# Performance work log

Measured on AMD Instinct MI355X. Metric: run time of the kernel, lower is better.

The kernel has to match this reference:

```python
import jax, jax.numpy as jnp
import numpy as np

HEADS = 16
D_MODEL = 1024
GROUP = 4
SEQ = 2048
HEAD_DIM = D_MODEL // HEADS          # 64
KV_HEADS = HEADS // GROUP            # 4


def rope_tables(head_dim, seq_len, base=10000.0):
    # NOTE: faithful to source: exp = -2*arange(0,d,2)/d  (steps of 2 -> base^{-4j/d})
    exp = -2.0 * jnp.arange(0, head_dim, 2, dtype=jnp.float32) / head_dim
    thetas = jnp.power(base, exp)                       # [d/2]
    m = jnp.arange(seq_len, dtype=jnp.float32)          # [S]
    freq = jnp.outer(m, thetas)                         # [S, d/2]
    return jnp.cos(freq), jnp.sin(freq)


def apply_rope(x, cos, sin):
    # x: [B,S,H,D]; complex rotation on consecutive pairs
    B, S, H, D = x.shape
    xr = x.reshape(B, S, H, D // 2, 2)
    x0, x1 = xr[..., 0], xr[..., 1]
    c = cos[None, :S, None, :]
    s = sin[None, :S, None, :]
    out = jnp.stack([x0 * c - x1 * s, x0 * s + x1 * c], axis=-1)
    return out.reshape(B, S, H, D)


def setup_inputs() -> dict:
    key = jax.random.key(0)
    ks = jax.random.split(key, 8)
    B = 1
    q = jax.random.normal(ks[0], (B, SEQ, D_MODEL), dtype=jnp.float32)
    k = jax.random.normal(ks[1], (B, SEQ, D_MODEL), dtype=jnp.float32)
    v = jax.random.normal(ks[2], (B, SEQ, D_MODEL), dtype=jnp.float32)
    mask = jnp.tril(jnp.ones((SEQ, SEQ), dtype=jnp.int32))[None]  # causal [B,S,S]
    sc = 0.02
    Wq = jax.random.normal(ks[3], (D_MODEL, D_MODEL), dtype=jnp.float32) * sc
    Wk = jax.random.normal(ks[4], (D_MODEL, D_MODEL // GROUP), dtype=jnp.float32) * sc
    Wv = jax.random.normal(ks[5], (D_MODEL, D_MODEL // GROUP), dtype=jnp.float32) * sc
    Wo = jax.random.normal(ks[6], (D_MODEL, D_MODEL), dtype=jnp.float32) * sc
    bq = jnp.zeros((D_MODEL,), jnp.float32)
    bk = jnp.zeros((D_MODEL // GROUP,), jnp.float32)
    bv = jnp.zeros((D_MODEL // GROUP,), jnp.float32)
    bo = jnp.zeros((D_MODEL,), jnp.float32)
    return {"q": q, "k": k, "v": v, "mask": mask, "Wq": Wq, "bq": bq,
            "Wk": Wk, "bk": bk, "Wv": Wv, "bv": bv, "Wo": Wo, "bo": bo}


def reference(q, k, v, mask, Wq, bq, Wk, bk, Wv, bv, Wo, bo):
    B, S, _ = q.shape
    cos, sin = rope_tables(HEAD_DIM, S)
    qh = (q @ Wq + bq).reshape(B, S, HEADS, HEAD_DIM)
    kh = (k @ Wk + bk).reshape(B, S, KV_HEADS, HEAD_DIM)
    vh = (v @ Wv + bv).reshape(B, S, KV_HEADS, HEAD_DIM)
    qh = apply_rope(qh, cos, sin)
    kh = apply_rope(kh, cos, sin)
    qh = qh.transpose(0, 2, 1, 3)                       # [B,H,S,D]
    kh = kh.transpose(0, 2, 1, 3)                       # [B,Hkv,S,D]
    vh = vh.transpose(0, 2, 1, 3)
    # torch .repeat tiles: query head j attends kv head j % KV_HEADS
    kh = jnp.tile(kh, (1, GROUP, 1, 1))                 # [B,H,S,D]
    vh = jnp.tile(vh, (1, GROUP, 1, 1))
    scores = jnp.einsum('bhqd,bhkd->bhqk', qh, kh) / jnp.sqrt(
        jnp.asarray(HEAD_DIM, dtype=qh.dtype))
    scores = jnp.where(mask[:, None, :, :] == 0, -jnp.inf, scores)
    attn = jax.nn.softmax(scores, axis=-1)
    out = jnp.einsum('bhqk,bhkd->bhqd', attn, vh)
    out = out.transpose(0, 2, 1, 3).reshape(B, S, D_MODEL)
    return out @ Wo + bo
```

## Files before the change

kernel.cpp:

```cpp
#include <hip/hip_runtime.h>
#include <hip/hip_bf16.h>
#include <math.h>


#define SEQ 2048
#define DM 1024
#define HD 64

using u16 = unsigned short;
typedef __attribute__((ext_vector_type(8))) short bf16x8;
typedef __attribute__((ext_vector_type(4))) float f32x4;

#define QSCALE 0.18033688011112042f

__device__ __forceinline__ u16 f2b(float f) {
    union { float f; unsigned int i; } v; v.f = f;
    unsigned int u = v.i;
    return (u16)((u + 0x7fffu + ((u >> 16) & 1u)) >> 16);
}
__device__ __forceinline__ u16 f2b_fast(float f) {
    union { float f; unsigned int i; } v; v.f = f;
    return (u16)((v.i + 0x8000u) >> 16);
}

__global__ __launch_bounds__(256) void prep_kernel(
    const float* __restrict__ qin, const float* __restrict__ kin, const float* __restrict__ vin,
    const float* __restrict__ Wq, const float* __restrict__ Wk,
    const float* __restrict__ Wv, const float* __restrict__ Wo,
    u16* __restrict__ Xq, u16* __restrict__ Xk, u16* __restrict__ Xv,
    u16* __restrict__ Wt, u16* __restrict__ wot, float2* __restrict__ rope)
{
    const int b = blockIdx.x;
    const int t = threadIdx.x;

    if (b < 640) {
        __shared__ short T[64][72];
        const float* W; u16* dst; int N, t0, rowoff;
        if (b < 256)      { W = Wq; dst = Wt;  N = 1024; t0 = b;       rowoff = 0; }
        else if (b < 320) { W = Wk; dst = Wt;  N = 256;  t0 = b - 256; rowoff = 1024; }
        else if (b < 384) { W = Wv; dst = Wt;  N = 256;  t0 = b - 320; rowoff = 1280; }
        else              { W = Wo; dst = wot; N = 1024; t0 = b - 384; rowoff = 0; }
        const int ntn = N >> 6;
        const int k0 = (t0 / ntn) * 64, n0 = (t0 % ntn) * 64;
        const int r = t >> 4, c4 = (t & 15) * 4;
        #pragma unroll
        for (int rr = 0; rr < 4; ++rr) {
            const int k = r + rr * 16;
            float4 w4 = *reinterpret_cast<const float4*>(W + (size_t)(k0 + k) * N + n0 + c4);
            T[c4 + 0][k] = (short)f2b(w4.x);
            T[c4 + 1][k] = (short)f2b(w4.y);
            T[c4 + 2][k] = (short)f2b(w4.z);
            T[c4 + 3][k] = (short)f2b(w4.w);
        }
        __syncthreads();
        const int n = t >> 2, ck = (t & 3) * 16;
        if (b < 384) {
            const int nt = (rowoff + n0) >> 6, kt = k0 >> 6;
            char* dp = (char*)(dst + (size_t)(nt * 16 + kt) * 4096) + n * 128;
            const int g0 = (t & 3) * 2, rx = n & 7;
            *reinterpret_cast<bf16x8*>(dp + (((g0    ) ^ rx) << 4)) =
                *reinterpret_cast<const bf16x8*>(&T[n][ck]);
            *reinterpret_cast<bf16x8*>(dp + (((g0 + 1) ^ rx) << 4)) =
                *reinterpret_cast<const bf16x8*>(&T[n][ck + 8]);
        } else {
            u16* dp = dst + (size_t)(n0 + n) * DM + k0 + ck;
            *reinterpret_cast<bf16x8*>(dp)     = *reinterpret_cast<const bf16x8*>(&T[n][ck]);
            *reinterpret_cast<bf16x8*>(dp + 8) = *reinterpret_cast<const bf16x8*>(&T[n][ck + 8]);
        }
    } else if (b < 1408) {
        const int idx = b - 640;
        const int which = idx >> 8;
        const int ib = idx & 255;
        const float* src = (which == 0) ? qin : (which == 1) ? kin : vin;
        u16* dst = (which == 0) ? Xq : (which == 1) ? Xk : Xv;
        const int m  = ib * 8 + (t >> 5);
        const int mt = m >> 6, r = m & 63, rx = r & 7;
        const int col0 = (t & 31) * 32;
        const float* sp = src + (size_t)m * 1024 + col0;
        #pragma unroll
        for (int c = 0; c < 4; ++c) {
            float4 x0 = *reinterpret_cast<const float4*>(sp + c * 8);
            float4 x1 = *reinterpret_cast<const float4*>(sp + c * 8 + 4);
            bf16x8 o;
            o[0] = (short)f2b(x0.x); o[1] = (short)f2b(x0.y);
            o[2] = (short)f2b(x0.z); o[3] = (short)f2b(x0.w);
            o[4] = (short)f2b(x1.x); o[5] = (short)f2b(x1.y);
            o[6] = (short)f2b(x1.z); o[7] = (short)f2b(x1.w);
            const int col = col0 + c * 8;
            const int kt = col >> 6, g = (col & 63) >> 3;
            char* dp = (char*)(dst + (size_t)(mt * 16 + kt) * 4096)
                     + r * 128 + ((g ^ rx) << 4);
            *reinterpret_cast<bf16x8*>(dp) = o;
        }
    } else {
        const int m = (b - 1408) * 256 + t;
        float2* rp = rope + (size_t)m * 32;
        for (int pi = 0; pi < 32; ++pi) {
            const float theta = exp2f(-0.8304820237f * (float)pi);
            float sn, cs;
            sincosf((float)m * theta, &sn, &cs);
            rp[pi] = make_float2(cs, sn);
        }
    }
}

__global__ __launch_bounds__(256) void proj_mfma(
    const u16* __restrict__ Xq, const u16* __restrict__ Xk, const u16* __restrict__ Xv,
    const u16* __restrict__ Wt,
    const float* __restrict__ bq, const float* __restrict__ bk, const float* __restrict__ bv,
    const float2* __restrict__ rope,
    u16* __restrict__ Qr, u16* __restrict__ Kr, u16* __restrict__ Vrt)
{
    const int n0 = blockIdx.x * 64, m0 = blockIdx.y * 64;
    const int zone = (n0 < 1024) ? 0 : (n0 < 1280) ? 1 : 2;
    const u16* __restrict__ Az = (zone == 0) ? Xq : (zone == 1) ? Xk : Xv;

    __shared__ __align__(16) u16 As[2][4096];
    __shared__ __align__(16) u16 Bs[2][4096];

    const int t = threadIdx.x;
    const int w = t >> 6, lane = t & 63, lm = lane & 15, quad = lane >> 4;

    f32x4 acc[4] = { {0,0,0,0}, {0,0,0,0}, {0,0,0,0}, {0,0,0,0} };

    const char* Ag = (const char*)(Az + (size_t)(m0 >> 6) * 16 * 4096);
    const char* Bg = (const char*)(Wt + (size_t)(n0 >> 6) * 16 * 4096);

    auto stage = [&](int bufi, int kti) {
        const char* gA = Ag + (size_t)kti * 8192 + w * 2048 + lane * 16;
        const char* gB = Bg + (size_t)kti * 8192 + w * 2048 + lane * 16;
        char* lA = (char*)&As[bufi][0] + w * 2048;
        char* lB = (char*)&Bs[bufi][0] + w * 2048;
        #pragma unroll
        for (int i = 0; i < 2; ++i) {
            __builtin_amdgcn_global_load_lds(
                (const __attribute__((address_space(1))) unsigned int*)(gA + i * 1024),
                (__attribute__((address_space(3))) unsigned int*)(lA + i * 1024), 16, 0, 0);
            __builtin_amdgcn_global_load_lds(
                (const __attribute__((address_space(1))) unsigned int*)(gB + i * 1024),
                (__attribute__((address_space(3))) unsigned int*)(lB + i * 1024), 16, 0, 0);
        }
    };

    stage(0, 0);
    __syncthreads();

    const int rA = 16 * w + lm;
    const int axr = rA & 7;
    for (int kt = 0; kt < 16; ++kt) {
        const int buf = kt & 1;
        if (kt < 15) stage(buf ^ 1, kt + 1);
        const char* Ab = (const char*)&As[buf][0];
        const char* Bb = (const char*)&Bs[buf][0];
        bf16x8 af0 = *reinterpret_cast<const bf16x8*>(Ab + rA * 128 + (((quad    ) ^ axr) << 4));
        bf16x8 af1 = *reinterpret_cast<const bf16x8*>(Ab + rA * 128 + (((4 | quad) ^ axr) << 4));
        #pragma unroll
        for (int nb = 0; nb < 4; ++nb) {
            const int rB = 16 * nb + lm, bxr = rB & 7;
            bf16x8 b0 = *reinterpret_cast<const bf16x8*>(Bb + rB * 128 + (((quad    ) ^ bxr) << 4));
            bf16x8 b1 = *reinterpret_cast<const bf16x8*>(Bb + rB * 128 + (((4 | quad) ^ bxr) << 4));
            acc[nb] = __builtin_amdgcn_mfma_f32_16x16x32_bf16(af0, b0, acc[nb], 0, 0, 0);
            acc[nb] = __builtin_amdgcn_mfma_f32_16x16x32_bf16(af1, b1, acc[nb], 0, 0, 0);
        }
        __syncthreads();
    }

    const float* __restrict__ bias = (zone == 0) ? bq : (zone == 1) ? bk : bv;
    const int nbase = (zone == 0) ? n0 : (zone == 1) ? (n0 - 1024) : (n0 - 1280);
    const int head = nbase >> 6;
    #pragma unroll
    for (int nb = 0; nb < 4; ++nb) {
        const int d = 16 * nb + lm;
        const float bvv = bias[nbase + d];
        float vals[4];
        #pragma unroll
        for (int r = 0; r < 4; ++r) vals[r] = acc[nb][r] + bvv;
        if (zone != 2) {
            const int pi = d >> 1;
            const bool odd = (lm & 1);
            const float sca = (zone == 0) ? QSCALE : 1.0f;
            u16* op = (zone == 0 ? Qr : Kr) + (size_t)head * SEQ * HD;
            #pragma unroll
            for (int r = 0; r < 4; ++r) {
                const int m = m0 + 16 * w + quad * 4 + r;
                const float2 cs2 = rope[(size_t)m * 32 + pi];
                float x  = vals[r];
                float xp = __shfl_xor(x, 1);
                float o  = (odd ? (xp * cs2.y + x * cs2.x)
                                : (x * cs2.x - xp * cs2.y)) * sca;
                op[(size_t)m * HD + d] = f2b(o);
            }
        } else {
            u16* vp = Vrt + ((size_t)head * HD + d) * SEQ;
            #pragma unroll
            for (int r = 0; r < 4; ++r) {
                const int m = m0 + 16 * w + quad * 4 + r;
                const int within = m & 63;
                const int pos = (m & ~63) + 4 * (within & 15) + (within >> 4);
                vp[pos] = f2b(vals[r]);
            }
        }
    }
}

__global__ __launch_bounds__(256) void attn_mfma(
    const u16* __restrict__ Qr, const u16* __restrict__ Kr, const u16* __restrict__ Vrt,
    u16* __restrict__ AO)
{
    const int bid = blockIdx.x;
    const int h  = bid & 15;
    const int qt = (bid < 256) ? (bid >> 4) : 31 - ((bid - 256) >> 4);
    const int kvh = h & 3;

    __shared__ u16 Ks[2][64][72];
    __shared__ u16 Vt[2][64][72];
    __shared__ u16 Ps[4][16][76];

    const int t = threadIdx.x;
    const int w = t >> 6, lane = t & 63, lm = lane & 15, quad = lane >> 4;

    {
        const int row = lane >> 2, c = (lane & 3) * 16;
        const u16* qp = Qr + ((size_t)h * SEQ + qt * 64 + w * 16 + row) * HD + c;
        *reinterpret_cast<bf16x8*>(&Ps[w][row][c])     = *reinterpret_cast<const bf16x8*>(qp);
        *reinterpret_cast<bf16x8*>(&Ps[w][row][c + 8]) = *reinterpret_cast<const bf16x8*>(qp + 8);
    }
    const bf16x8 aq0 = *reinterpret_cast<const bf16x8*>(&Ps[w][lm][quad * 8]);
    const bf16x8 aq1 = *reinterpret_cast<const bf16x8*>(&Ps[w][lm][32 + quad * 8]);

    f32x4 O[4] = { {0,0,0,0}, {0,0,0,0}, {0,0,0,0}, {0,0,0,0} };
    float lp[4] = { 0.f, 0.f, 0.f, 0.f };

    const int srow = t >> 2, sc2 = (t & 3) * 16;
    const u16* kb_ = Kr  + ((size_t)kvh * SEQ + srow) * HD + sc2;
    const u16* vb_ = Vrt + ((size_t)kvh * HD + srow) * SEQ + sc2;
    bf16x8 kR0 = *reinterpret_cast<const bf16x8*>(kb_);
    bf16x8 kR1 = *reinterpret_cast<const bf16x8*>(kb_ + 8);
    bf16x8 vR0 = *reinterpret_cast<const bf16x8*>(vb_);
    bf16x8 vR1 = *reinterpret_cast<const bf16x8*>(vb_ + 8);

    for (int kt = 0; kt <= qt; ++kt) {
        const int buf = kt & 1;
        *reinterpret_cast<bf16x8*>(&Ks[buf][srow][sc2])     = kR0;
        *reinterpret_cast<bf16x8*>(&Ks[buf][srow][sc2 + 8]) = kR1;
        *reinterpret_cast<bf16x8*>(&Vt[buf][srow][sc2])     = vR0;
        *reinterpret_cast<bf16x8*>(&Vt[buf][srow][sc2 + 8]) = vR1;
        if (kt < qt) {
            kR0 = *reinterpret_cast<const bf16x8*>(kb_ + (size_t)(kt + 1) * 64 * HD);
            kR1 = *reinterpret_cast<const bf16x8*>(kb_ + (size_t)(kt + 1) * 64 * HD + 8);
            vR0 = *reinterpret_cast<const bf16x8*>(vb_ + (size_t)(kt + 1) * 64);
            vR1 = *reinterpret_cast<const bf16x8*>(vb_ + (size_t)(kt + 1) * 64 + 8);
        }
        __syncthreads();

        f32x4 s[4];
        #pragma unroll
        for (int nb = 0; nb < 4; ++nb) {
            bf16x8 b0 = *reinterpret_cast<const bf16x8*>(&Ks[buf][16 * nb + lm][quad * 8]);
            bf16x8 b1 = *reinterpret_cast<const bf16x8*>(&Ks[buf][16 * nb + lm][32 + quad * 8]);
            f32x4 zz = { 0.f, 0.f, 0.f, 0.f };
            zz = __builtin_amdgcn_mfma_f32_16x16x32_bf16(aq0, b0, zz, 0, 0, 0);
            s[nb] = __builtin_amdgcn_mfma_f32_16x16x32_bf16(aq1, b1, zz, 0, 0, 0);
        }

        if (kt == qt) {
            #pragma unroll
            for (int nb = 0; nb < 4; ++nb)
                #pragma unroll
                for (int r = 0; r < 4; ++r)
                    if (16 * nb + lm > 16 * w + quad * 4 + r) s[nb][r] = -INFINITY;
        }

        #pragma unroll
        for (int r = 0; r < 4; ++r) {
            u16 pk[4];
            #pragma unroll
            for (int nb = 0; nb < 4; ++nb) {
                float e = __builtin_amdgcn_exp2f(fminf(s[nb][r], 126.f));
                lp[r] += e;
                pk[nb] = f2b_fast(e);
            }
            *reinterpret_cast<uint2*>(&Ps[w][quad * 4 + r][4 * lm]) =
                *reinterpret_cast<uint2*>(pk);
        }

        const bf16x8 ap0 = *reinterpret_cast<const bf16x8*>(&Ps[w][lm][quad * 8]);
        const bf16x8 ap1 = *reinterpret_cast<const bf16x8*>(&Ps[w][lm][32 + quad * 8]);
        #pragma unroll
        for (int db = 0; db < 4; ++db) {
            bf16x8 v0 = *reinterpret_cast<const bf16x8*>(&Vt[buf][16 * db + lm][quad * 8]);
            bf16x8 v1 = *reinterpret_cast<const bf16x8*>(&Vt[buf][16 * db + lm][32 + quad * 8]);
            O[db] = __builtin_amdgcn_mfma_f32_16x16x32_bf16(ap0, v0, O[db], 0, 0, 0);
            O[db] = __builtin_amdgcn_mfma_f32_16x16x32_bf16(ap1, v1, O[db], 0, 0, 0);
        }
    }

    #pragma unroll
    for (int r = 0; r < 4; ++r) {
        #pragma unroll
        for (int off = 1; off < 16; off <<= 1)
            lp[r] += __shfl_xor(lp[r], off);
        const float inv = 1.0f / lp[r];
        const size_t row = (size_t)(qt * 64 + 16 * w + quad * 4 + r) * DM + (size_t)h * HD;
        #pragma unroll
        for (int db = 0; db < 4; ++db)
            AO[row + 16 * db + lm] = f2b(O[db][r] * inv);
    }
}

__global__ __launch_bounds__(256) void oproj_mfma(
    const u16* __restrict__ AO, const u16* __restrict__ wot,
    const float* __restrict__ bo, float* __restrict__ out)
{
    __shared__ short As[2][64][72];
    __shared__ short Bs[2][64][72];
    const int t = threadIdx.x;
    const int w = t >> 6, lane = t & 63, lm = lane & 15, quad = lane >> 4;
    const int m0 = blockIdx.y * 64, n0 = blockIdx.x * 64;
    const int sr = t >> 2, sc = (t & 3) * 16;

    f32x4 acc[4] = { {0,0,0,0}, {0,0,0,0}, {0,0,0,0}, {0,0,0,0} };

    const u16* ap_ = AO  + (size_t)(m0 + sr) * DM + sc;
    const u16* bp_ = wot + (size_t)(n0 + sr) * DM + sc;
    bf16x8 aR0 = *reinterpret_cast<const bf16x8*>(ap_);
    bf16x8 aR1 = *reinterpret_cast<const bf16x8*>(ap_ + 8);
    bf16x8 bR0 = *reinterpret_cast<const bf16x8*>(bp_);
    bf16x8 bR1 = *reinterpret_cast<const bf16x8*>(bp_ + 8);

    for (int k0 = 0; k0 < DM; k0 += 64) {
        const int buf = (k0 >> 6) & 1;
        *reinterpret_cast<bf16x8*>(&As[buf][sr][sc])     = aR0;
        *reinterpret_cast<bf16x8*>(&As[buf][sr][sc + 8]) = aR1;
        *reinterpret_cast<bf16x8*>(&Bs[buf][sr][sc])     = bR0;
        *reinterpret_cast<bf16x8*>(&Bs[buf][sr][sc + 8]) = bR1;
        if (k0 + 64 < DM) {
            aR0 = *reinterpret_cast<const bf16x8*>(ap_ + k0 + 64);
            aR1 = *reinterpret_cast<const bf16x8*>(ap_ + k0 + 72);
            bR0 = *reinterpret_cast<const bf16x8*>(bp_ + k0 + 64);
            bR1 = *reinterpret_cast<const bf16x8*>(bp_ + k0 + 72);
        }
        __syncthreads();
        bf16x8 af0 = *reinterpret_cast<const bf16x8*>(&As[buf][16 * w + lm][quad * 8]);
        bf16x8 af1 = *reinterpret_cast<const bf16x8*>(&As[buf][16 * w + lm][32 + quad * 8]);
        #pragma unroll
        for (int nb = 0; nb < 4; ++nb) {
            bf16x8 b0 = *reinterpret_cast<const bf16x8*>(&Bs[buf][16 * nb + lm][quad * 8]);
            bf16x8 b1 = *reinterpret_cast<const bf16x8*>(&Bs[buf][16 * nb + lm][32 + quad * 8]);
            acc[nb] = __builtin_amdgcn_mfma_f32_16x16x32_bf16(af0, b0, acc[nb], 0, 0, 0);
            acc[nb] = __builtin_amdgcn_mfma_f32_16x16x32_bf16(af1, b1, acc[nb], 0, 0, 0);
        }
        __syncthreads();
    }

    #pragma unroll
    for (int nb = 0; nb < 4; ++nb) {
        const int dl = 16 * nb + lm;
        const float bv = bo[n0 + dl];
        #pragma unroll
        for (int r = 0; r < 4; ++r) {
            const int m = m0 + 16 * w + quad * 4 + r;
            out[(size_t)m * DM + n0 + dl] = acc[nb][r] + bv;
        }
    }
}

extern "C" void kernel_launch(void* const* d_in, const int* in_sizes, int n_in,
                              void* d_out, int out_size, void* d_ws, size_t ws_size,
                              hipStream_t stream)
{
    const float* q  = (const float*)d_in[0];
    const float* k  = (const float*)d_in[1];
    const float* v  = (const float*)d_in[2];
    const float* Wq = (const float*)d_in[4];
    const float* bq = (const float*)d_in[5];
    const float* Wk = (const float*)d_in[6];
    const float* bk = (const float*)d_in[7];
    const float* Wv = (const float*)d_in[8];
    const float* bv = (const float*)d_in[9];
    const float* Wo = (const float*)d_in[10];
    const float* bo = (const float*)d_in[11];
    float* out = (float*)d_out;

    u16* Xq  = (u16*)d_ws;
    u16* Xk  = Xq  + (size_t)SEQ * DM;
    u16* Xv  = Xk  + (size_t)SEQ * DM;
    u16* Wt  = Xv  + (size_t)SEQ * DM;
    u16* wot = Wt  + (size_t)1536 * 1024;
    u16* Qr  = wot + (size_t)1024 * 1024;
    u16* Kr  = Qr  + (size_t)16 * SEQ * HD;
    u16* Vrt = Kr  + (size_t)4 * SEQ * HD;
    u16* AO  = Vrt + (size_t)4 * SEQ * HD;
    float2* rope = (float2*)(AO + (size_t)SEQ * DM);

    hipLaunchKernelGGL(prep_kernel, dim3(1416), dim3(256), 0, stream,
                       q, k, v, Wq, Wk, Wv, Wo, Xq, Xk, Xv, Wt, wot, rope);
    hipLaunchKernelGGL(proj_mfma, dim3(24, 32), dim3(256), 0, stream,
                       Xq, Xk, Xv, Wt, bq, bk, bv, rope, Qr, Kr, Vrt);
    hipLaunchKernelGGL(attn_mfma, dim3(512), dim3(256), 0, stream,
                       Qr, Kr, Vrt, AO);
    hipLaunchKernelGGL(oproj_mfma, dim3(16, 32), dim3(256), 0, stream,
                       AO, wot, bo, out);
}
```

Before: 165.4 us.

## Share async-LDS GEMM core with deeper prefetch; tile AO and Wo for o-proj

```diff
diff --git a/kernel.cpp b/kernel.cpp
--- a/kernel.cpp
+++ b/kernel.cpp
@@ -22,6 +22,11 @@
     union { float f; unsigned int i; } v; v.f = f;
     return (u16)((v.i + 0x8000u) >> 16);
 }
+
+#define VMCNT4 do { asm volatile("s_waitcnt vmcnt(4)" ::: "memory"); \
+                    __builtin_amdgcn_sched_barrier(0); } while (0)
+#define VMCNT0 do { asm volatile("s_waitcnt vmcnt(0)" ::: "memory"); \
+                    __builtin_amdgcn_sched_barrier(0); } while (0)
 
 __global__ __launch_bounds__(256) void prep_kernel(
     const float* __restrict__ qin, const float* __restrict__ kin, const float* __restrict__ vin,
@@ -54,19 +59,13 @@
         }
         __syncthreads();
         const int n = t >> 2, ck = (t & 3) * 16;
-        if (b < 384) {
-            const int nt = (rowoff + n0) >> 6, kt = k0 >> 6;
-            char* dp = (char*)(dst + (size_t)(nt * 16 + kt) * 4096) + n * 128;
-            const int g0 = (t & 3) * 2, rx = n & 7;
-            *reinterpret_cast<bf16x8*>(dp + (((g0    ) ^ rx) << 4)) =
-                *reinterpret_cast<const bf16x8*>(&T[n][ck]);
-            *reinterpret_cast<bf16x8*>(dp + (((g0 + 1) ^ rx) << 4)) =
-                *reinterpret_cast<const bf16x8*>(&T[n][ck + 8]);
-        } else {
-            u16* dp = dst + (size_t)(n0 + n) * DM + k0 + ck;
-            *reinterpret_cast<bf16x8*>(dp)     = *reinterpret_cast<const bf16x8*>(&T[n][ck]);
-            *reinterpret_cast<bf16x8*>(dp + 8) = *reinterpret_cast<const bf16x8*>(&T[n][ck + 8]);
-        }
+        const int nt = (rowoff + n0) >> 6, kt = k0 >> 6;
+        char* dp = (char*)(dst + (size_t)(nt * 16 + kt) * 4096) + n * 128;
+        const int g0 = (t & 3) * 2, rx = n & 7;
+        *reinterpret_cast<bf16x8*>(dp + (((g0    ) ^ rx) << 4)) =
+            *reinterpret_cast<const bf16x8*>(&T[n][ck]);
+        *reinterpret_cast<bf16x8*>(dp + (((g0 + 1) ^ rx) << 4)) =
+            *reinterpret_cast<const bf16x8*>(&T[n][ck + 8]);
     } else if (b < 1408) {
         const int idx = b - 640;
         const int which = idx >> 8;
@@ -104,27 +103,14 @@
     }
 }
 
-__global__ __launch_bounds__(256) void proj_mfma(
-    const u16* __restrict__ Xq, const u16* __restrict__ Xk, const u16* __restrict__ Xv,
-    const u16* __restrict__ Wt,
-    const float* __restrict__ bq, const float* __restrict__ bk, const float* __restrict__ bv,
-    const float2* __restrict__ rope,
-    u16* __restrict__ Qr, u16* __restrict__ Kr, u16* __restrict__ Vrt)
-{
-    const int n0 = blockIdx.x * 64, m0 = blockIdx.y * 64;
-    const int zone = (n0 < 1024) ? 0 : (n0 < 1280) ? 1 : 2;
-    const u16* __restrict__ Az = (zone == 0) ? Xq : (zone == 1) ? Xk : Xv;
-
-    __shared__ __align__(16) u16 As[2][4096];
-    __shared__ __align__(16) u16 Bs[2][4096];
-
-    const int t = threadIdx.x;
+template <typename EPI>
+__device__ __forceinline__ void gemm64_core(
+    const char* Ag, const char* Bg, u16 (*As)[4096], u16 (*Bs)[4096],
+    int t, EPI&& epilogue)
+{
     const int w = t >> 6, lane = t & 63, lm = lane & 15, quad = lane >> 4;
 
     f32x4 acc[4] = { {0,0,0,0}, {0,0,0,0}, {0,0,0,0}, {0,0,0,0} };
-
-    const char* Ag = (const char*)(Az + (size_t)(m0 >> 6) * 16 * 4096);
-    const char* Bg = (const char*)(Wt + (size_t)(n0 >> 6) * 16 * 4096);
 
     auto stage = [&](int bufi, int kti) {
         const char* gA = Ag + (size_t)kti * 8192 + w * 2048 + lane * 16;
@@ -143,13 +129,15 @@
     };
 
     stage(0, 0);
-    __syncthreads();
+    stage(1, 1);
 
     const int rA = 16 * w + lm;
     const int axr = rA & 7;
     for (int kt = 0; kt < 16; ++kt) {
         const int buf = kt & 1;
-        if (kt < 15) stage(buf ^ 1, kt + 1);
+        if (kt < 15) { VMCNT4; } else { VMCNT0; }
+        __builtin_amdgcn_s_barrier();
+        __builtin_amdgcn_sched_barrier(0);
         const char* Ab = (const char*)&As[buf][0];
         const char* Bb = (const char*)&Bs[buf][0];
         bf16x8 af0 = *reinterpret_cast<const bf16x8*>(Ab + rA * 128 + (((quad    ) ^ axr) << 4));
@@ -162,45 +150,69 @@
             acc[nb] = __builtin_amdgcn_mfma_f32_16x16x32_bf16(af0, b0, acc[nb], 0, 0, 0);
             acc[nb] = __builtin_amdgcn_mfma_f32_16x16x32_bf16(af1, b1, acc[nb], 0, 0, 0);
         }
-        __syncthreads();
-    }
-
-    const float* __restrict__ bias = (zone == 0) ? bq : (zone == 1) ? bk : bv;
-    const int nbase = (zone == 0) ? n0 : (zone == 1) ? (n0 - 1024) : (n0 - 1280);
-    const int head = nbase >> 6;
-    #pragma unroll
-    for (int nb = 0; nb < 4; ++nb) {
-        const int d = 16 * nb + lm;
-        const float bvv = bias[nbase + d];
-        float vals[4];
-        #pragma unroll
-        for (int r = 0; r < 4; ++r) vals[r] = acc[nb][r] + bvv;
-        if (zone != 2) {
-            const int pi = d >> 1;
-            const bool odd = (lm & 1);
-            const float sca = (zone == 0) ? QSCALE : 1.0f;
-            u16* op = (zone == 0 ? Qr : Kr) + (size_t)head * SEQ * HD;
+        __builtin_amdgcn_sched_barrier(0);
+        __builtin_amdgcn_s_barrier();
+        if (kt < 14) stage(buf, kt + 2);
+    }
+    epilogue(acc, w, lm, quad);
+}
+
+__global__ __launch_bounds__(256) void proj_mfma(
+    const u16* __restrict__ Xq, const u16* __restrict__ Xk, const u16* __restrict__ Xv,
+    const u16* __restrict__ Wt,
+    const float* __restrict__ bq, const float* __restrict__ bk, const float* __restrict__ bv,
+    const float2* __restrict__ rope,
+    u16* __restrict__ Qr, u16* __restrict__ Kr, u16* __restrict__ Vrt)
+{
+    const int n0 = blockIdx.x * 64, m0 = blockIdx.y * 64;
+    const int zone = (n0 < 1024) ? 0 : (n0 < 1280) ? 1 : 2;
+    const u16* __restrict__ Az = (zone == 0) ? Xq : (zone == 1) ? Xk : Xv;
+
+    __shared__ __align__(16) u16 As[2][4096];
+    __shared__ __align__(16) u16 Bs[2][4096];
+
+    const char* Ag = (const char*)(Az + (size_t)(m0 >> 6) * 16 * 4096);
+    const char* Bg = (const char*)(Wt + (size_t)(n0 >> 6) * 16 * 4096);
+
+    gemm64_core(Ag, Bg, As, Bs, threadIdx.x,
+        [&](f32x4 (&acc)[4], int w, int lm, int quad) {
+            const float* __restrict__ bias = (zone == 0) ? bq : (zone == 1) ? bk : bv;
+            const int nbase = (zone == 0) ? n0 : (zone == 1) ? (n0 - 1024) : (n0 - 1280);
+            const int head = nbase >> 6;
             #pragma unroll
-            for (int r = 0; r < 4; ++r) {
-                const int m = m0 + 16 * w + quad * 4 + r;
-                const float2 cs2 = rope[(size_t)m * 32 + pi];
-                float x  = vals[r];
-                float xp = __shfl_xor(x, 1);
-                float o  = (odd ? (xp * cs2.y + x * cs2.x)
-                                : (x * cs2.x - xp * cs2.y)) * sca;
-                op[(size_t)m * HD + d] = f2b(o);
+            for (int nb = 0; nb < 4; ++nb) {
+                const int d = 16 * nb + lm;
+                const float bvv = bias[nbase + d];
+                float vals[4];
+                #pragma unroll
+                for (int r = 0; r < 4; ++r) vals[r] = acc[nb][r] + bvv;
+                if (zone != 2) {
+                    const int pi = d >> 1;
+                    const bool odd = (lm & 1);
+                    const float sca = (zone == 0) ? QSCALE : 1.0f;
+                    u16* op = (zone == 0 ? Qr : Kr) + (size_t)head * SEQ * HD;
+                    #pragma unroll
+                    for (int r = 0; r < 4; ++r) {
+                        const int m = m0 + 16 * w + quad * 4 + r;
+                        const float2 cs2 = rope[(size_t)m * 32 + pi];
+                        float x  = vals[r];
+                        float xp = __shfl_xor(x, 1);
+                        float o  = (odd ? (xp * cs2.y + x * cs2.x)
+                                        : (x * cs2.x - xp * cs2.y)) * sca;
+                        op[(size_t)m * HD + d] = f2b(o);
+                    }
+                } else {
+                    u16* vp = Vrt + ((size_t)head * HD + d) * SEQ;
+                    #pragma unroll
+                    for (int r = 0; r < 4; ++r) {
+                        const int m = m0 + 16 * w + quad * 4 + r;
+                        const int within = m & 63;
+                        const int pos = (m & ~63) + 4 * (within & 15) + (within >> 4);
+                        vp[pos] = f2b(vals[r]);
+                    }
+                }
             }
-        } else {
-            u16* vp = Vrt + ((size_t)head * HD + d) * SEQ;
-            #pragma unroll
-            for (int r = 0; r < 4; ++r) {
-                const int m = m0 + 16 * w + quad * 4 + r;
-                const int within = m & 63;
-                const int pos = (m & ~63) + 4 * (within & 15) + (within >> 4);
-                vp[pos] = f2b(vals[r]);
-            }
-        }
-    }
+        });
 }
 
 __global__ __launch_bounds__(256) void attn_mfma(
@@ -254,6 +266,7 @@
         __syncthreads();
 
         f32x4 s[4];
+        __builtin_amdgcn_s_setprio(1);
         #pragma unroll
         for (int nb = 0; nb < 4; ++nb) {
             bf16x8 b0 = *reinterpret_cast<const bf16x8*>(&Ks[buf][16 * nb + lm][quad * 8]);
@@ -262,6 +275,7 @@
             zz = __builtin_amdgcn_mfma_f32_16x16x32_bf16(aq0, b0, zz, 0, 0, 0);
             s[nb] = __builtin_amdgcn_mfma_f32_16x16x32_bf16(aq1, b1, zz, 0, 0, 0);
         }
+        __builtin_amdgcn_s_setprio(0);
 
         if (kt == qt) {
             #pragma unroll
@@ -286,6 +300,7 @@
 
         const bf16x8 ap0 = *reinterpret_cast<const bf16x8*>(&Ps[w][lm][quad * 8]);
         const bf16x8 ap1 = *reinterpret_cast<const bf16x8*>(&Ps[w][lm][32 + quad * 8]);
+        __builtin_amdgcn_s_setprio(1);
         #pragma unroll
         for (int db = 0; db < 4; ++db) {
             bf16x8 v0 = *reinterpret_cast<const bf16x8*>(&Vt[buf][16 * db + lm][quad * 8]);
@@ -293,6 +308,7 @@
             O[db] = __builtin_amdgcn_mfma_f32_16x16x32_bf16(ap0, v0, O[db], 0, 0, 0);
             O[db] = __builtin_amdgcn_mfma_f32_16x16x32_bf16(ap1, v1, O[db], 0, 0, 0);
         }
+        __builtin_amdgcn_s_setprio(0);
     }
 
     #pragma unroll
@@ -301,10 +317,15 @@
         for (int off = 1; off < 16; off <<= 1)
             lp[r] += __shfl_xor(lp[r], off);
         const float inv = 1.0f / lp[r];
-        const size_t row = (size_t)(qt * 64 + 16 * w + quad * 4 + r) * DM + (size_t)h * HD;
-        #pragma unroll
-        for (int db = 0; db < 4; ++db)
-            AO[row + 16 * db + lm] = f2b(O[db][r] * inv);
+        const int r_in = 16 * w + quad * 4 + r;
+        const int rx = r_in & 7;
+        u16* tp = AO + (size_t)(qt * 16 + h) * 4096 + r_in * 64;
+        #pragma unroll
+        for (int db = 0; db < 4; ++db) {
+            const int c = 16 * db + lm;
+            const int g = (c >> 3);
+            tp[((g ^ rx) << 3) + (c & 7)] = f2b(O[db][r] * inv);
+        }
     }
 }
 
@@ -312,57 +333,26 @@
     const u16* __restrict__ AO, const u16* __restrict__ wot,
     const float* __restrict__ bo, float* __restrict__ out)
 {
-    __shared__ short As[2][64][72];
-    __shared__ short Bs[2][64][72];
-    const int t = threadIdx.x;
-    const int w = t >> 6, lane = t & 63, lm = lane & 15, quad = lane >> 4;
+    __shared__ __align__(16) u16 As[2][4096];
+    __shared__ __align__(16) u16 Bs[2][4096];
     const int m0 = blockIdx.y * 64, n0 = blockIdx.x * 64;
-    const int sr = t >> 2, sc = (t & 3) * 16;
-
-    f32x4 acc[4] = { {0,0,0,0}, {0,0,0,0}, {0,0,0,0}, {0,0,0,0} };
-
-    const u16* ap_ = AO  + (size_t)(m0 + sr) * DM + sc;
-    const u16* bp_ = wot + (size_t)(n0 + sr) * DM + sc;
-    bf16x8 aR0 = *reinterpret_cast<const bf16x8*>(ap_);
-    bf16x8 aR1 = *reinterpret_cast<const bf16x8*>(ap_ + 8);
-    bf16x8 bR0 = *reinterpret_cast<const bf16x8*>(bp_);
-    bf16x8 bR1 = *reinterpret_cast<const bf16x8*>(bp_ + 8);
-
-    for (int k0 = 0; k0 < DM; k0 += 64) {
-        const int buf = (k0 >> 6) & 1;
-        *reinterpret_cast<bf16x8*>(&As[buf][sr][sc])     = aR0;
-        *reinterpret_cast<bf16x8*>(&As[buf][sr][sc + 8]) = aR1;
-        *reinterpret_cast<bf16x8*>(&Bs[buf][sr][sc])     = bR0;
-        *reinterpret_cast<bf16x8*>(&Bs[buf][sr][sc + 8]) = bR1;
-        if (k0 + 64 < DM) {
-            aR0 = *reinterpret_cast<const bf16x8*>(ap_ + k0 + 64);
-            aR1 = *reinterpret_cast<const bf16x8*>(ap_ + k0 + 72);
-            bR0 = *reinterpret_cast<const bf16x8*>(bp_ + k0 + 64);
-            bR1 = *reinterpret_cast<const bf16x8*>(bp_ + k0 + 72);
-        }
-        __syncthreads();
-        bf16x8 af0 = *reinterpret_cast<const bf16x8*>(&As[buf][16 * w + lm][quad * 8]);
-        bf16x8 af1 = *reinterpret_cast<const bf16x8*>(&As[buf][16 * w + lm][32 + quad * 8]);
-        #pragma unroll
-        for (int nb = 0; nb < 4; ++nb) {
-            bf16x8 b0 = *reinterpret_cast<const bf16x8*>(&Bs[buf][16 * nb + lm][quad * 8]);
-            bf16x8 b1 = *reinterpret_cast<const bf16x8*>(&Bs[buf][16 * nb + lm][32 + quad * 8]);
-            acc[nb] = __builtin_amdgcn_mfma_f32_16x16x32_bf16(af0, b0, acc[nb], 0, 0, 0);
-            acc[nb] = __builtin_amdgcn_mfma_f32_16x16x32_bf16(af1, b1, acc[nb], 0, 0, 0);
-        }
-        __syncthreads();
-    }
-
-    #pragma unroll
-    for (int nb = 0; nb < 4; ++nb) {
-        const int dl = 16 * nb + lm;
-        const float bv = bo[n0 + dl];
-        #pragma unroll
-        for (int r = 0; r < 4; ++r) {
-            const int m = m0 + 16 * w + quad * 4 + r;
-            out[(size_t)m * DM + n0 + dl] = acc[nb][r] + bv;
-        }
-    }
+
+    const char* Ag = (const char*)(AO  + (size_t)(m0 >> 6) * 16 * 4096);
+    const char* Bg = (const char*)(wot + (size_t)(n0 >> 6) * 16 * 4096);
+
+    gemm64_core(Ag, Bg, As, Bs, threadIdx.x,
+        [&](f32x4 (&acc)[4], int w, int lm, int quad) {
+            #pragma unroll
+            for (int nb = 0; nb < 4; ++nb) {
+                const int dl = 16 * nb + lm;
+                const float bv = bo[n0 + dl];
+                #pragma unroll
+                for (int r = 0; r < 4; ++r) {
+                    const int m = m0 + 16 * w + quad * 4 + r;
+                    out[(size_t)m * DM + n0 + dl] = acc[nb][r] + bv;
+                }
+            }
+        });
 }
 
 extern "C" void kernel_launch(void* const* d_in, const int* in_sizes, int n_in,
```

Measured after the change: 177.3 us. 1.07x slower.
